# Kernel tuning notes

Measured on AMD Instinct MI355X. Metric: run time of the kernel, lower is better.

The kernel has to match this reference:

```python
import jax, jax.numpy as jnp
import numpy as np

NUM_OBS_OS = 8
NUM_OBS_TS = 6
HIDDEN = 128
NUM_ACTIONS = 9
B = 32768
N_TS = 32


def setup_inputs() -> dict:
    key = jax.random.key(0)
    ks = jax.random.split(key, 16)
    s_OS = jax.random.normal(ks[0], (B, NUM_OBS_OS), dtype=jnp.float32)
    s_TS = jax.random.normal(ks[1], (B, N_TS, NUM_OBS_TS), dtype=jnp.float32)
    # variable number of valid target ships per row (0..N_TS); trailing slots -> NaN
    lengths = jax.random.randint(ks[2], (B,), 0, N_TS + 1)
    pad = jnp.arange(N_TS)[None, :] >= lengths[:, None]          # [B, N_TS]
    s_TS = jnp.where(pad[:, :, None], jnp.nan, s_TS)
    s = jnp.concatenate([s_OS, s_TS.reshape(B, N_TS * NUM_OBS_TS)], axis=1)

    def lin(k, out_d, in_d):
        bound = 1.0 / np.sqrt(in_d)
        kw, kb = jax.random.split(k)
        W = jax.random.uniform(kw, (out_d, in_d), jnp.float32, -bound, bound)
        b = jax.random.uniform(kb, (out_d,), jnp.float32, -bound, bound)
        return W, b

    W_os, b_os = lin(ks[3], HIDDEN, NUM_OBS_OS)
    bound = 1.0 / np.sqrt(HIDDEN)
    W_ih = jax.random.uniform(ks[4], (4 * HIDDEN, NUM_OBS_TS), jnp.float32, -bound, bound)
    W_hh = jax.random.uniform(ks[5], (4 * HIDDEN, HIDDEN), jnp.float32, -bound, bound)
    b_ih = jax.random.uniform(ks[6], (4 * HIDDEN,), jnp.float32, -bound, bound)
    b_hh = jax.random.uniform(ks[7], (4 * HIDDEN,), jnp.float32, -bound, bound)
    W_ts, b_ts = lin(ks[8], HIDDEN, HIDDEN)
    W_c1, b_c1 = lin(ks[9], HIDDEN, 2 * HIDDEN)
    W_c2, b_c2 = lin(ks[10], NUM_ACTIONS, HIDDEN)
    return {"s": s, "W_os": W_os, "b_os": b_os, "W_ih": W_ih, "W_hh": W_hh,
            "b_ih": b_ih, "b_hh": b_hh, "W_ts": W_ts, "b_ts": b_ts,
            "W_c1": W_c1, "b_c1": b_c1, "W_c2": W_c2, "b_c2": b_c2}


def _lstm(x, W_ih, W_hh, b_ih, b_hh):
    """Single-layer batch-first LSTM; x: [B, T, I] -> outputs [B, T, H]."""
    Bc, T, _ = x.shape
    H = W_hh.shape[1]
    # precompute input projections for all steps: [T, B, 4H]
    xg = jnp.einsum('bti,gi->tbg', x, W_ih) + (b_ih + b_hh)

    def step(carry, xt):
        h, c = carry
        gates = xt + h @ W_hh.T                      # [B, 4H]
        i, f, g, o = jnp.split(gates, 4, axis=-1)    # torch order: i, f, g, o
        i = jax.nn.sigmoid(i)
        f = jax.nn.sigmoid(f)
        g = jnp.tanh(g)
        o = jax.nn.sigmoid(o)
        c = f * c + i * g
        h = o * jnp.tanh(c)
        return (h, c), h

    h0 = jnp.zeros((Bc, H), x.dtype)
    c0 = jnp.zeros((Bc, H), x.dtype)
    _, hs = jax.lax.scan(step, (h0, c0), xg)         # hs: [T, B, H]
    return jnp.transpose(hs, (1, 0, 2))


def reference(s, W_os, b_os, W_ih, W_hh, b_ih, b_hh, W_ts, b_ts, W_c1, b_c1, W_c2, b_c2):
    Bc = s.shape[0]
    s_OS = s[:, :NUM_OBS_OS]
    s_TS = s[:, NUM_OBS_OS:].reshape(Bc, -1, NUM_OBS_TS)          # [B, N_TS, 6]
    valid = jnp.logical_not(jnp.isnan(s_TS[:, :, 0]))             # [B, N_TS]
    n_obs = jnp.sum(valid, axis=1)                                # [B]
    h_idx = jnp.maximum(n_obs, 1) - 1                             # last valid step
    s_TS = jnp.where(jnp.isnan(s_TS), 0.0, s_TS)

    x_OS = jax.nn.relu(s_OS @ W_os.T + b_os)                      # [B, 128]

    out = _lstm(s_TS, W_ih, W_hh, b_ih, b_hh)                     # [B, N_TS, 128]
    x_TS = jnp.take_along_axis(out, h_idx[:, None, None], axis=1)[:, 0]  # [B, 128]
    x_TS = jnp.where((n_obs == 0)[:, None], 0.0, x_TS)
    x_TS = jax.nn.relu(x_TS @ W_ts.T + b_ts)

    x = jnp.concatenate([x_OS, x_TS], axis=1)                     # [B, 256]
    x = jax.nn.relu(x @ W_c1.T + b_c1)
    return x @ W_c2.T + b_c2                                      # [B, num_actions]
```

## Files before the change

kernel.cpp:

```cpp
#include <hip/hip_runtime.h>

#define NOBS_OS 8
#define NOBS_TS 6
#define HID 128
#define NACT 9
#define BTOT 32768
#define NTS 32
#define ROWS 16
#define NTILES 2048
#define QUADS 512
#define BLOCK 512
#define PREB 128

#define LEN_OFF 0
#define PERM_OFF BTOT
#define HIST_OFF (2 * BTOT)

typedef __attribute__((ext_vector_type(8))) short short8;
typedef __attribute__((ext_vector_type(4))) float f32x4;

__device__ inline unsigned pkbf(float a, float b) {
  unsigned r;
  asm("v_cvt_pk_bf16_f32 %0, %1, %2" : "=v"(r) : "v"(a), "v"(b));
  return r;
}

__device__ inline float fexp2(float x) {
#if defined(__has_builtin) && __has_builtin(__builtin_amdgcn_exp2f)
  return __builtin_amdgcn_exp2f(x);
#else
  return exp2f(x);
#endif
}
__device__ inline float frcp_(float x) {
#if defined(__has_builtin) && __has_builtin(__builtin_amdgcn_rcpf)
  return __builtin_amdgcn_rcpf(x);
#else
  return 1.0f / x;
#endif
}

__device__ inline short8 pack8(f32x4 a, f32x4 b) {
  union { unsigned u[4]; short8 s; } r;
  r.u[0] = pkbf(a[0], a[1]); r.u[1] = pkbf(a[2], a[3]);
  r.u[2] = pkbf(b[0], b[1]); r.u[3] = pkbf(b[2], b[3]);
  return r.s;
}

__device__ inline short8 pack8s(const float* p, float s) {
  union { unsigned u[4]; short8 r; } r;
#pragma unroll
  for (int i = 0; i < 4; ++i) r.u[i] = pkbf(p[2 * i] * s, p[2 * i + 1] * s);
  return r.r;
}

__global__ void count_kernel(const float* __restrict__ s, int* __restrict__ ws) {
  __shared__ int lh[NTS + 1];
  const int tid = threadIdx.x;
  if (tid <= NTS) lh[tid] = 0;
  __syncthreads();
  const int row = blockIdx.x * 256 + tid;
  const float* p = s + (size_t)row * 200 + NOBS_OS;
  int lo = 0, hi = NTS;
  while (lo < hi) {
    const int mid = (lo + hi) >> 1;
    const float v = p[mid * NOBS_TS];
    if (v == v) lo = mid + 1; else hi = mid;
  }
  ws[LEN_OFF + row] = lo;
  atomicAdd(&lh[lo], 1);
  __syncthreads();
  if (tid <= NTS) ws[HIST_OFF + blockIdx.x * (NTS + 1) + tid] = lh[tid];
}

__global__ void scatter_kernel(int* __restrict__ ws) {
  __shared__ int tot[NTS + 1], pre[NTS + 1], gb[NTS + 1], lh[NTS + 1];
  const int tid = threadIdx.x;
  if (tid <= NTS) {
    int t = 0, pr = 0;
    for (int k = 0; k < PREB; ++k) {
      const int h = ws[HIST_OFF + k * (NTS + 1) + tid];
      t += h;
      if (k < (int)blockIdx.x) pr += h;
    }
    tot[tid] = t;
    pre[tid] = pr;
    lh[tid] = 0;
  }
  __syncthreads();
  if (tid == 0) {
    int a = 0;
    for (int b = 0; b <= NTS; ++b) { gb[b] = a; a += tot[b]; }
  }
  __syncthreads();
  const int row = blockIdx.x * 256 + tid;
  const int len = ws[LEN_OFF + row];
  const int r = atomicAdd(&lh[len], 1);
  __syncthreads();
  ws[PERM_OFF + gb[len] + pre[len] + r] = row;
}


#define GX(CN, T)                                                            \
  {                                                                          \
    short8 ax = z8;                                                          \
    if (q == 0) ax = *(const short8*)&x_st[CN][c * 264 + (T) * 8];           \
    _Pragma("unroll") for (int a = 0; a < 4; ++a)                            \
        acc[CN][a] = __builtin_amdgcn_mfma_f32_16x16x32_bf16(                \
            ax, Bh[a][4], biasv[a], 0, 0, 0);                                \
  }

#define GH(CN, T)                                                            \
  {                                                                          \
    const unsigned short* hb = hA[CN][((T) + 1) & 1];                        \
    _Pragma("unroll") for (int kt = 0; kt < 4; ++kt) {                       \
      const short8 ah = *(const short8*)&hb[kt * 512 + L * 8];               \
      _Pragma("unroll") for (int a = 0; a < 4; ++a)                          \
          acc[CN][a] = __builtin_amdgcn_mfma_f32_16x16x32_bf16(              \
              ah, Bh[a][kt], acc[CN][a], 0, 0, 0);                           \
    }                                                                        \
  }

#define ACT(CN, T)                                                           \
  {                                                                          \
    unsigned short* hw = &hA[CN][(T) & 1][pbase];                            \
    float hv[4];                                                             \
    _Pragma("unroll") for (int r = 0; r < 4; ++r) {                          \
      const float ei = fexp2(acc[CN][0][r]);                                 \
      const float ef = fexp2(acc[CN][1][r]);                                 \
      const float eg = fexp2(acc[CN][2][r]);                                 \
      const float eo = fexp2(acc[CN][3][r]);                                 \
      const float P = (1.0f + ei) * (1.0f + eg);                             \
      const float fp = 1.0f + ef;                                            \
      const float num = cc[CN][r] * P + (1.0f - eg) * fp;                    \
      const float cv = num * frcp_(fp * P);                                  \
      cc[CN][r] = cv;                                                        \
      const float ec = fexp2(cv * -2.88539008f);                             \
      const float roc = frcp_((1.0f + eo) * (1.0f + ec));                    \
      hv[r] = (1.0f - ec) * roc;                                             \
    }                                                                        \
    const unsigned p01 = pkbf(hv[0], hv[1]);                                 \
    const unsigned p23 = pkbf(hv[2], hv[3]);                                 \
    hw[0] = (unsigned short)p01;                                             \
    hw[8] = (unsigned short)(p01 >> 16);                                     \
    hw[16] = (unsigned short)p23;                                            \
    hw[24] = (unsigned short)(p23 >> 16);                                    \
    _Pragma("unroll") for (int r = 0; r < 4; ++r) {                          \
      if (((tpck[CN] >> (r * 8)) & 255u) == (unsigned)(T))                   \
        xts[CN][r] = hv[r];                                                  \
    }                                                                        \
  }

__global__ __launch_bounds__(BLOCK, 2) void recdqn_kernel(
    const float* __restrict__ s, const float* __restrict__ W_os,
    const float* __restrict__ b_os, const float* __restrict__ W_ih,
    const float* __restrict__ W_hh, const float* __restrict__ b_ih,
    const float* __restrict__ b_hh, const float* __restrict__ W_ts,
    const float* __restrict__ b_ts, const float* __restrict__ W_c1,
    const float* __restrict__ b_c1, const float* __restrict__ W_c2,
    const float* __restrict__ b_c2, const int* __restrict__ ws,
    float* __restrict__ out) {
  __shared__ unsigned short x_st[4][ROWS * 264];
  __shared__ unsigned short hA[4][2][2048];
  __shared__ unsigned short xtsb[4][2048];
  __shared__ int n_lds[4][ROWS];
  __shared__ int rid_s[4][ROWS];
  __shared__ int tmax_sh[4];
  unsigned short* xcat_al = &hA[0][0][0];
  unsigned short* x2b_al = &xtsb[0][0];

  const int tid = threadIdx.x;
  const int L = tid & 63;
  const int w = tid >> 6;
  const int c = L & 15;
  const int q = L >> 4;
  const int j = (w << 4) | c;

  const short8 z8 = {0, 0, 0, 0, 0, 0, 0, 0};

  short8 Bh[4][5];
  f32x4 biasv[4];
#pragma unroll
  for (int a = 0; a < 4; ++a) {
    const float sc = (a == 2) ? -2.88539008f : -1.44269504f;
    const int n = (a << 7) + j;
    const float bb = sc * (b_ih[n] + b_hh[n]);
    f32x4 bv = {bb, bb, bb, bb};
    biasv[a] = bv;
#pragma unroll
    for (int kt = 0; kt < 4; ++kt)
      Bh[a][kt] = pack8s(W_hh + n * HID + kt * 32 + q * 8, sc);
    short8 fx = z8;
    if (q == 0) {
      const float* px = W_ih + n * NOBS_TS;
      union { unsigned u[4]; short8 s; } fu;
      fu.u[0] = pkbf(px[0] * sc, px[1] * sc);
      fu.u[1] = pkbf(px[2] * sc, px[3] * sc);
      fu.u[2] = pkbf(px[4] * sc, px[5] * sc);
      fu.u[3] = 0;
      fx = fu.s;
    }
    Bh[a][4] = fx;
  }

  const int pbase = ((j >> 5) << 9) + (((j >> 3) & 3) << 7) + (q << 5) + (j & 7);

  const int p = (QUADS - 1) - blockIdx.x;
  if (tid < 64) {
    const int cn = tid >> 4, rr = tid & 15;
    const int row = ws[PERM_OFF + (4 * p + cn) * ROWS + rr];
    rid_s[cn][rr] = row;
    n_lds[cn][rr] = ws[LEN_OFF + row];
  }
  __syncthreads();

#pragma unroll
  for (int it = 0; it < 4; ++it) {
    const int slot = tid + it * 512;
    const int cn = slot >> 9, rt = slot & 511, r = rt >> 5, tq = rt & 31;
    short8 v = z8;
    if (tq < n_lds[cn][r]) {
      const float2* ps =
          (const float2*)(s + (size_t)rid_s[cn][r] * 200 + NOBS_OS + tq * NOBS_TS);
      const float2 A = ps[0], Bv = ps[1], Cv = ps[2];
      union { unsigned u[4]; short8 s; } vu;
      vu.u[0] = pkbf(A.x, A.y);
      vu.u[1] = pkbf(Bv.x, Bv.y);
      vu.u[2] = pkbf(Cv.x, Cv.y);
      vu.u[3] = 0;
      v = vu.s;
    }
    *(short8*)&x_st[cn][r * 264 + tq * 8] = v;
  }
  if (tid == 0) {
#pragma unroll
    for (int cn = 0; cn < 4; ++cn) {
      int mx = 0;
      for (int r = 0; r < ROWS; ++r) mx = max(mx, n_lds[cn][r]);
      tmax_sh[cn] = mx;
    }
  }
  __syncthreads();

  const int tm0 = tmax_sh[0], tm1 = tmax_sh[1];
  const int tm2 = tmax_sh[2], tm3 = tmax_sh[3];
  unsigned tpck[4];
#pragma unroll
  for (int cn = 0; cn < 4; ++cn) {
    unsigned pk = 0;
#pragma unroll
    for (int b = 0; b < 4; ++b)
      pk |= ((unsigned)((n_lds[cn][q * 4 + b] - 1) & 255)) << (b * 8);
    tpck[cn] = pk;
  }

  float cc[4][4], xts[4][4];
#pragma unroll
  for (int i = 0; i < 4; ++i) {
    cc[0][i] = 0.0f; cc[1][i] = 0.0f; cc[2][i] = 0.0f; cc[3][i] = 0.0f;
    xts[0][i] = 0.0f; xts[1][i] = 0.0f; xts[2][i] = 0.0f; xts[3][i] = 0.0f;
  }

  f32x4 acc[4][4];
  if (tm3 > 0) {
    if (tm0 > 0) GX(0, 0)
    if (tm1 > 0) GX(1, 0)
    if (tm2 > 0) GX(2, 0)
    GX(3, 0)
    if (tm0 > 0) ACT(0, 0)
    if (tm1 > 0) ACT(1, 0)
    if (tm2 > 0) ACT(2, 0)
    ACT(3, 0)
    __syncthreads();
    int t = 1;
    for (; t < tm0; ++t) {
      GX(0, t) GH(0, t)
      GX(1, t) GH(1, t)
      GX(2, t) GH(2, t)
      GX(3, t) GH(3, t)
      ACT(0, t) ACT(1, t) ACT(2, t) ACT(3, t)
      __syncthreads();
    }
    for (; t < tm1; ++t) {
      GX(1, t) GH(1, t)
      GX(2, t) GH(2, t)
      GX(3, t) GH(3, t)
      ACT(1, t) ACT(2, t) ACT(3, t)
      __syncthreads();
    }
    for (; t < tm2; ++t) {
      GX(2, t) GH(2, t)
      GX(3, t) GH(3, t)
      ACT(2, t) ACT(3, t)
      __syncthreads();
    }
    for (; t < tm3; ++t) {
      GX(3, t) GH(3, t)
      ACT(3, t)
      __syncthreads();
    }
  }

#pragma unroll
  for (int cn = 0; cn < 4; ++cn) {
    const unsigned p01 = pkbf(xts[cn][0], xts[cn][1]);
    const unsigned p23 = pkbf(xts[cn][2], xts[cn][3]);
    unsigned short* pw = &xtsb[cn][pbase];
    pw[0] = (unsigned short)p01;
    pw[8] = (unsigned short)(p01 >> 16);
    pw[16] = (unsigned short)p23;
    pw[24] = (unsigned short)(p23 >> 16);
  }
  __syncthreads();

  short8 Fts[4], Fc1[8], Fc2[4], bosf = z8;
#pragma unroll
  for (int kt = 0; kt < 4; ++kt) {
    const f32x4* pp = (const f32x4*)(W_ts + j * HID + kt * 32 + q * 8);
    Fts[kt] = pack8(pp[0], pp[1]);
  }
#pragma unroll
  for (int kt = 0; kt < 8; ++kt) {
    const f32x4* pp = (const f32x4*)(W_c1 + j * 256 + kt * 32 + q * 8);
    Fc1[kt] = pack8(pp[0], pp[1]);
  }
#pragma unroll
  for (int kt = 0; kt < 4; ++kt) Fc2[kt] = z8;
  if (w == 0 && c < NACT) {
#pragma unroll
    for (int kt = 0; kt < 4; ++kt) {
      const f32x4* pp = (const f32x4*)(W_c2 + c * HID + kt * 32 + q * 8);
      Fc2[kt] = pack8(pp[0], pp[1]);
    }
  }
  if (q == 0) {
    const f32x4* pb = (const f32x4*)(W_os + j * NOBS_OS);
    bosf = pack8(pb[0], pb[1]);
  }
  const float bts = b_ts[j], bc1 = b_c1[j], bos = b_os[j];
  const float bc2 = (w == 0 && c < NACT) ? b_c2[c] : 0.0f;

#pragma unroll
  for (int cn = 0; cn < 4; ++cn) {
    f32x4 a2 = {bts, bts, bts, bts};
#pragma unroll
    for (int kt = 0; kt < 4; ++kt) {
      const short8 af = *(const short8*)&xtsb[cn][kt * 512 + L * 8];
      a2 = __builtin_amdgcn_mfma_f32_16x16x32_bf16(af, Fts[kt], a2, 0, 0, 0);
    }
    const unsigned p01 = pkbf(fmaxf(a2[0], 0.0f), fmaxf(a2[1], 0.0f));
    const unsigned p23 = pkbf(fmaxf(a2[2], 0.0f), fmaxf(a2[3], 0.0f));
    unsigned short* xc = xcat_al + cn * 4096 + 2048 + pbase;
    xc[0] = (unsigned short)p01;
    xc[8] = (unsigned short)(p01 >> 16);
    xc[16] = (unsigned short)p23;
    xc[24] = (unsigned short)(p23 >> 16);
  }
#pragma unroll
  for (int cn = 0; cn < 4; ++cn) {
    short8 aos = z8;
    if (q == 0) {
      const f32x4* pa = (const f32x4*)(s + (size_t)rid_s[cn][c] * 200);
      aos = pack8(pa[0], pa[1]);
    }
    f32x4 a2 = {bos, bos, bos, bos};
    a2 = __builtin_amdgcn_mfma_f32_16x16x32_bf16(aos, bosf, a2, 0, 0, 0);
    const unsigned p01 = pkbf(fmaxf(a2[0], 0.0f), fmaxf(a2[1], 0.0f));
    const unsigned p23 = pkbf(fmaxf(a2[2], 0.0f), fmaxf(a2[3], 0.0f));
    unsigned short* xc = xcat_al + cn * 4096 + pbase;
    xc[0] = (unsigned short)p01;
    xc[8] = (unsigned short)(p01 >> 16);
    xc[16] = (unsigned short)p23;
    xc[24] = (unsigned short)(p23 >> 16);
  }
  __syncthreads();

#pragma unroll
  for (int cn = 0; cn < 4; ++cn) {
    f32x4 a2 = {bc1, bc1, bc1, bc1};
#pragma unroll
    for (int kt = 0; kt < 8; ++kt) {
      const short8 af = *(const short8*)&xcat_al[cn * 4096 + kt * 512 + L * 8];
      a2 = __builtin_amdgcn_mfma_f32_16x16x32_bf16(af, Fc1[kt], a2, 0, 0, 0);
    }
    const unsigned p01 = pkbf(fmaxf(a2[0], 0.0f), fmaxf(a2[1], 0.0f));
    const unsigned p23 = pkbf(fmaxf(a2[2], 0.0f), fmaxf(a2[3], 0.0f));
    unsigned short* xb = x2b_al + cn * 2048 + pbase;
    xb[0] = (unsigned short)p01;
    xb[8] = (unsigned short)(p01 >> 16);
    xb[16] = (unsigned short)p23;
    xb[24] = (unsigned short)(p23 >> 16);
  }
  __syncthreads();

  if (w == 0) {
#pragma unroll
    for (int cn = 0; cn < 4; ++cn) {
      f32x4 accf = {bc2, bc2, bc2, bc2};
#pragma unroll
      for (int kt = 0; kt < 4; ++kt) {
        const short8 af = *(const short8*)&x2b_al[cn * 2048 + kt * 512 + L * 8];
        accf = __builtin_amdgcn_mfma_f32_16x16x32_bf16(af, Fc2[kt], accf, 0, 0, 0);
      }
      if (c < NACT) {
#pragma unroll
        for (int r = 0; r < 4; ++r)
          out[(size_t)rid_s[cn][q * 4 + r] * NACT + c] = accf[r];
      }
    }
  }
}

extern "C" void kernel_launch(void* const* d_in, const int* in_sizes, int n_in,
                              void* d_out, int out_size, void* d_ws, size_t ws_size,
                              hipStream_t stream) {
  (void)in_sizes; (void)n_in; (void)out_size; (void)ws_size;
  const float* s    = (const float*)d_in[0];
  const float* W_os = (const float*)d_in[1];
  const float* b_os = (const float*)d_in[2];
  const float* W_ih = (const float*)d_in[3];
  const float* W_hh = (const float*)d_in[4];
  const float* b_ih = (const float*)d_in[5];
  const float* b_hh = (const float*)d_in[6];
  const float* W_ts = (const float*)d_in[7];
  const float* b_ts = (const float*)d_in[8];
  const float* W_c1 = (const float*)d_in[9];
  const float* b_c1 = (const float*)d_in[10];
  const float* W_c2 = (const float*)d_in[11];
  const float* b_c2 = (const float*)d_in[12];
  int* ws = (int*)d_ws;
  float* outp = (float*)d_out;

  count_kernel<<<PREB, 256, 0, stream>>>(s, ws);
  scatter_kernel<<<PREB, 256, 0, stream>>>(ws);
  recdqn_kernel<<<QUADS, BLOCK, 0, stream>>>(
      s, W_os, b_os, W_ih, W_hh, b_ih, b_hh, W_ts, b_ts, W_c1, b_c1, W_c2,
      b_c2, ws, outp);
}
```

Before: 231.6 us.

## Run eight interleaved LSTM chains per block and stream inputs from global

```diff
diff --git a/kernel.cpp b/kernel.cpp
--- a/kernel.cpp
+++ b/kernel.cpp
@@ -8,7 +8,8 @@
 #define NTS 32
 #define ROWS 16
 #define NTILES 2048
-#define QUADS 512
+#define CHAINS 8
+#define GRID 256
 #define BLOCK 512
 #define PREB 128
 
@@ -101,24 +102,51 @@
 }
 
 
-#define GX(CN, T)                                                            \
+#define GXL(CN, T)                                                           \
   {                                                                          \
-    short8 ax = z8;                                                          \
-    if (q == 0) ax = *(const short8*)&x_st[CN][c * 264 + (T) * 8];           \
-    _Pragma("unroll") for (int a = 0; a < 4; ++a)                            \
-        acc[CN][a] = __builtin_amdgcn_mfma_f32_16x16x32_bf16(                \
-            ax, Bh[a][4], biasv[a], 0, 0, 0);                                \
-  }
-
-#define GH(CN, T)                                                            \
+    axv##CN = z8;                                                            \
+    if (q == 0) {                                                            \
+      const float2* ps =                                                     \
+          (const float2*)(s + (size_t)ridr[CN] * 200 + NOBS_OS + (T) * NOBS_TS); \
+      const float2 A = ps[0], Bv = ps[1], Cv = ps[2];                        \
+      union { unsigned u[4]; short8 s8; } vu;                                \
+      vu.u[0] = pkbf(A.x, A.y);                                              \
+      vu.u[1] = pkbf(Bv.x, Bv.y);                                            \
+      vu.u[2] = pkbf(Cv.x, Cv.y);                                            \
+      vu.u[3] = 0;                                                           \
+      axv##CN = vu.s8;                                                       \
+    }                                                                        \
+  }
+
+#define GHF(CN, T)                                                           \
   {                                                                          \
     const unsigned short* hb = hA[CN][((T) + 1) & 1];                        \
-    _Pragma("unroll") for (int kt = 0; kt < 4; ++kt) {                       \
+    {                                                                        \
+      const short8 ah = *(const short8*)&hb[L * 8];                          \
+      _Pragma("unroll") for (int a = 0; a < 4; ++a)                          \
+          acc[(CN) & 3][a] = __builtin_amdgcn_mfma_f32_16x16x32_bf16(        \
+              ah, Bh[a][0], biasv[a], 0, 0, 0);                              \
+    }                                                                        \
+    _Pragma("unroll") for (int kt = 1; kt < 4; ++kt) {                       \
       const short8 ah = *(const short8*)&hb[kt * 512 + L * 8];               \
       _Pragma("unroll") for (int a = 0; a < 4; ++a)                          \
-          acc[CN][a] = __builtin_amdgcn_mfma_f32_16x16x32_bf16(              \
-              ah, Bh[a][kt], acc[CN][a], 0, 0, 0);                           \
+          acc[(CN) & 3][a] = __builtin_amdgcn_mfma_f32_16x16x32_bf16(        \
+              ah, Bh[a][kt], acc[(CN) & 3][a], 0, 0, 0);                     \
     }                                                                        \
+  }
+
+#define GXM(CN)                                                              \
+  {                                                                          \
+    _Pragma("unroll") for (int a = 0; a < 4; ++a)                            \
+        acc[(CN) & 3][a] = __builtin_amdgcn_mfma_f32_16x16x32_bf16(          \
+            axv##CN, Bh[a][4], acc[(CN) & 3][a], 0, 0, 0);                   \
+  }
+
+#define GX0(CN)                                                              \
+  {                                                                          \
+    _Pragma("unroll") for (int a = 0; a < 4; ++a)                            \
+        acc[(CN) & 3][a] = __builtin_amdgcn_mfma_f32_16x16x32_bf16(          \
+            axv##CN, Bh[a][4], biasv[a], 0, 0, 0);                           \
   }
 
 #define ACT(CN, T)                                                           \
@@ -126,10 +154,10 @@
     unsigned short* hw = &hA[CN][(T) & 1][pbase];                            \
     float hv[4];                                                             \
     _Pragma("unroll") for (int r = 0; r < 4; ++r) {                          \
-      const float ei = fexp2(acc[CN][0][r]);                                 \
-      const float ef = fexp2(acc[CN][1][r]);                                 \
-      const float eg = fexp2(acc[CN][2][r]);                                 \
-      const float eo = fexp2(acc[CN][3][r]);                                 \
+      const float ei = fexp2(acc[(CN) & 3][0][r]);                           \
+      const float ef = fexp2(acc[(CN) & 3][1][r]);                           \
+      const float eg = fexp2(acc[(CN) & 3][2][r]);                           \
+      const float eo = fexp2(acc[(CN) & 3][3][r]);                           \
       const float P = (1.0f + ei) * (1.0f + eg);                             \
       const float fp = 1.0f + ef;                                            \
       const float num = cc[CN][r] * P + (1.0f - eg) * fp;                    \
@@ -141,14 +169,19 @@
     }                                                                        \
     const unsigned p01 = pkbf(hv[0], hv[1]);                                 \
     const unsigned p23 = pkbf(hv[2], hv[3]);                                 \
-    hw[0] = (unsigned short)p01;                                             \
-    hw[8] = (unsigned short)(p01 >> 16);                                     \
-    hw[16] = (unsigned short)p23;                                            \
-    hw[24] = (unsigned short)(p23 >> 16);                                    \
-    _Pragma("unroll") for (int r = 0; r < 4; ++r) {                          \
-      if (((tpck[CN] >> (r * 8)) & 255u) == (unsigned)(T))                   \
-        xts[CN][r] = hv[r];                                                  \
-    }                                                                        \
+    const unsigned short hb16_0 = (unsigned short)p01;                       \
+    const unsigned short hb16_1 = (unsigned short)(p01 >> 16);               \
+    const unsigned short hb16_2 = (unsigned short)p23;                       \
+    const unsigned short hb16_3 = (unsigned short)(p23 >> 16);               \
+    hw[0] = hb16_0;                                                          \
+    hw[8] = hb16_1;                                                          \
+    hw[16] = hb16_2;                                                         \
+    hw[24] = hb16_3;                                                         \
+    unsigned short* xw = &xtsb[CN][pbase];                                   \
+    if (((tpck[CN] >> 0) & 255u) == (unsigned)(T)) xw[0] = hb16_0;           \
+    if (((tpck[CN] >> 8) & 255u) == (unsigned)(T)) xw[8] = hb16_1;           \
+    if (((tpck[CN] >> 16) & 255u) == (unsigned)(T)) xw[16] = hb16_2;         \
+    if (((tpck[CN] >> 24) & 255u) == (unsigned)(T)) xw[24] = hb16_3;         \
   }
 
 __global__ __launch_bounds__(BLOCK, 2) void recdqn_kernel(
@@ -160,12 +193,11 @@
     const float* __restrict__ b_c1, const float* __restrict__ W_c2,
     const float* __restrict__ b_c2, const int* __restrict__ ws,
     float* __restrict__ out) {
-  __shared__ unsigned short x_st[4][ROWS * 264];
-  __shared__ unsigned short hA[4][2][2048];
-  __shared__ unsigned short xtsb[4][2048];
-  __shared__ int n_lds[4][ROWS];
-  __shared__ int rid_s[4][ROWS];
-  __shared__ int tmax_sh[4];
+  __shared__ unsigned short hA[CHAINS][2][2048];
+  __shared__ unsigned short xtsb[CHAINS][2048];
+  __shared__ int n_lds[CHAINS][ROWS];
+  __shared__ int rid_s[CHAINS][ROWS];
+  __shared__ int tmax_sh[CHAINS];
   unsigned short* xcat_al = &hA[0][0][0];
   unsigned short* x2b_al = &xtsb[0][0];
 
@@ -193,125 +225,98 @@
     short8 fx = z8;
     if (q == 0) {
       const float* px = W_ih + n * NOBS_TS;
-      union { unsigned u[4]; short8 s; } fu;
+      union { unsigned u[4]; short8 s8; } fu;
       fu.u[0] = pkbf(px[0] * sc, px[1] * sc);
       fu.u[1] = pkbf(px[2] * sc, px[3] * sc);
       fu.u[2] = pkbf(px[4] * sc, px[5] * sc);
       fu.u[3] = 0;
-      fx = fu.s;
+      fx = fu.s8;
     }
     Bh[a][4] = fx;
   }
 
   const int pbase = ((j >> 5) << 9) + (((j >> 3) & 3) << 7) + (q << 5) + (j & 7);
 
-  const int p = (QUADS - 1) - blockIdx.x;
-  if (tid < 64) {
+  if (tid < CHAINS * ROWS) {
     const int cn = tid >> 4, rr = tid & 15;
-    const int row = ws[PERM_OFF + (4 * p + cn) * ROWS + rr];
+    const int row = ws[PERM_OFF + ((int)blockIdx.x + 256 * cn) * ROWS + rr];
     rid_s[cn][rr] = row;
     n_lds[cn][rr] = ws[LEN_OFF + row];
   }
-  __syncthreads();
-
-#pragma unroll
-  for (int it = 0; it < 4; ++it) {
-    const int slot = tid + it * 512;
-    const int cn = slot >> 9, rt = slot & 511, r = rt >> 5, tq = rt & 31;
-    short8 v = z8;
-    if (tq < n_lds[cn][r]) {
-      const float2* ps =
-          (const float2*)(s + (size_t)rid_s[cn][r] * 200 + NOBS_OS + tq * NOBS_TS);
-      const float2 A = ps[0], Bv = ps[1], Cv = ps[2];
-      union { unsigned u[4]; short8 s; } vu;
-      vu.u[0] = pkbf(A.x, A.y);
-      vu.u[1] = pkbf(Bv.x, Bv.y);
-      vu.u[2] = pkbf(Cv.x, Cv.y);
-      vu.u[3] = 0;
-      v = vu.s;
-    }
-    *(short8*)&x_st[cn][r * 264 + tq * 8] = v;
-  }
-  if (tid == 0) {
-#pragma unroll
-    for (int cn = 0; cn < 4; ++cn) {
-      int mx = 0;
-      for (int r = 0; r < ROWS; ++r) mx = max(mx, n_lds[cn][r]);
-      tmax_sh[cn] = mx;
-    }
-  }
-  __syncthreads();
-
-  const int tm0 = tmax_sh[0], tm1 = tmax_sh[1];
-  const int tm2 = tmax_sh[2], tm3 = tmax_sh[3];
-  unsigned tpck[4];
-#pragma unroll
-  for (int cn = 0; cn < 4; ++cn) {
+  {
+    short8* xz = (short8*)&xtsb[0][0];
+#pragma unroll
+    for (int i2 = 0; i2 < 4; ++i2) xz[tid + i2 * 512] = z8;
+  }
+  __syncthreads();
+  if (tid < CHAINS) {
+    int mx = 0;
+    for (int r = 0; r < ROWS; ++r) mx = max(mx, n_lds[tid][r]);
+    tmax_sh[tid] = mx;
+  }
+  __syncthreads();
+
+  const int tm0 = tmax_sh[0], tm1 = tmax_sh[1], tm2 = tmax_sh[2],
+            tm3 = tmax_sh[3], tm4 = tmax_sh[4], tm5 = tmax_sh[5],
+            tm6 = tmax_sh[6], tm7 = tmax_sh[7];
+  unsigned tpck[CHAINS];
+  int ridr[CHAINS];
+#pragma unroll
+  for (int cn = 0; cn < CHAINS; ++cn) {
     unsigned pk = 0;
 #pragma unroll
     for (int b = 0; b < 4; ++b)
       pk |= ((unsigned)((n_lds[cn][q * 4 + b] - 1) & 255)) << (b * 8);
     tpck[cn] = pk;
-  }
-
-  float cc[4][4], xts[4][4];
-#pragma unroll
-  for (int i = 0; i < 4; ++i) {
-    cc[0][i] = 0.0f; cc[1][i] = 0.0f; cc[2][i] = 0.0f; cc[3][i] = 0.0f;
-    xts[0][i] = 0.0f; xts[1][i] = 0.0f; xts[2][i] = 0.0f; xts[3][i] = 0.0f;
-  }
+    ridr[cn] = rid_s[cn][c];
+  }
+
+  float cc[CHAINS][4];
+#pragma unroll
+  for (int cn = 0; cn < CHAINS; ++cn)
+#pragma unroll
+    for (int i = 0; i < 4; ++i) cc[cn][i] = 0.0f;
 
   f32x4 acc[4][4];
-  if (tm3 > 0) {
-    if (tm0 > 0) GX(0, 0)
-    if (tm1 > 0) GX(1, 0)
-    if (tm2 > 0) GX(2, 0)
-    GX(3, 0)
+  short8 axv0, axv1, axv2, axv3, axv4, axv5, axv6, axv7;
+  if (tm7 > 0) {
+    if (tm0 > 0) { GXL(0, 0) GX0(0) }
+    if (tm1 > 0) { GXL(1, 0) GX0(1) }
+    if (tm2 > 0) { GXL(2, 0) GX0(2) }
+    if (tm3 > 0) { GXL(3, 0) GX0(3) }
     if (tm0 > 0) ACT(0, 0)
     if (tm1 > 0) ACT(1, 0)
     if (tm2 > 0) ACT(2, 0)
-    ACT(3, 0)
+    if (tm3 > 0) ACT(3, 0)
+    if (tm4 > 0) { GXL(4, 0) GX0(4) }
+    if (tm5 > 0) { GXL(5, 0) GX0(5) }
+    if (tm6 > 0) { GXL(6, 0) GX0(6) }
+    { GXL(7, 0) GX0(7) }
+    if (tm4 > 0) ACT(4, 0)
+    if (tm5 > 0) ACT(5, 0)
+    if (tm6 > 0) ACT(6, 0)
+    ACT(7, 0)
     __syncthreads();
-    int t = 1;
-    for (; t < tm0; ++t) {
-      GX(0, t) GH(0, t)
-      GX(1, t) GH(1, t)
-      GX(2, t) GH(2, t)
-      GX(3, t) GH(3, t)
-      ACT(0, t) ACT(1, t) ACT(2, t) ACT(3, t)
+    for (int t = 1; t < tm7; ++t) {
+      if (t < tm0) { GXL(0, t) GHF(0, t) GXM(0) }
+      if (t < tm1) { GXL(1, t) GHF(1, t) GXM(1) }
+      if (t < tm2) { GXL(2, t) GHF(2, t) GXM(2) }
+      if (t < tm3) { GXL(3, t) GHF(3, t) GXM(3) }
+      if (t < tm0) ACT(0, t)
+      if (t < tm1) ACT(1, t)
+      if (t < tm2) ACT(2, t)
+      if (t < tm3) ACT(3, t)
+      if (t < tm4) { GXL(4, t) GHF(4, t) GXM(4) }
+      if (t < tm5) { GXL(5, t) GHF(5, t) GXM(5) }
+      if (t < tm6) { GXL(6, t) GHF(6, t) GXM(6) }
+      { GXL(7, t) GHF(7, t) GXM(7) }
+      if (t < tm4) ACT(4, t)
+      if (t < tm5) ACT(5, t)
+      if (t < tm6) ACT(6, t)
+      ACT(7, t)
       __syncthreads();
     }
-    for (; t < tm1; ++t) {
-      GX(1, t) GH(1, t)
-      GX(2, t) GH(2, t)
-      GX(3, t) GH(3, t)
-      ACT(1, t) ACT(2, t) ACT(3, t)
-      __syncthreads();
-    }
-    for (; t < tm2; ++t) {
-      GX(2, t) GH(2, t)
-      GX(3, t) GH(3, t)
-      ACT(2, t) ACT(3, t)
-      __syncthreads();
-    }
-    for (; t < tm3; ++t) {
-      GX(3, t) GH(3, t)
-      ACT(3, t)
-      __syncthreads();
-    }
-  }
-
-#pragma unroll
-  for (int cn = 0; cn < 4; ++cn) {
-    const unsigned p01 = pkbf(xts[cn][0], xts[cn][1]);
-    const unsigned p23 = pkbf(xts[cn][2], xts[cn][3]);
-    unsigned short* pw = &xtsb[cn][pbase];
-    pw[0] = (unsigned short)p01;
-    pw[8] = (unsigned short)(p01 >> 16);
-    pw[16] = (unsigned short)p23;
-    pw[24] = (unsigned short)(p23 >> 16);
-  }
-  __syncthreads();
+  }
 
   short8 Fts[4], Fc1[8], Fc2[4], bosf = z8;
 #pragma unroll
@@ -341,7 +346,7 @@
   const float bc2 = (w == 0 && c < NACT) ? b_c2[c] : 0.0f;
 
 #pragma unroll
-  for (int cn = 0; cn < 4; ++cn) {
+  for (int cn = 0; cn < CHAINS; ++cn) {
     f32x4 a2 = {bts, bts, bts, bts};
 #pragma unroll
     for (int kt = 0; kt < 4; ++kt) {
@@ -357,7 +362,7 @@
     xc[24] = (unsigned short)(p23 >> 16);
   }
 #pragma unroll
-  for (int cn = 0; cn < 4; ++cn) {
+  for (int cn = 0; cn < CHAINS; ++cn) {
     short8 aos = z8;
     if (q == 0) {
       const f32x4* pa = (const f32x4*)(s + (size_t)rid_s[cn][c] * 200);
@@ -376,7 +381,7 @@
   __syncthreads();
 
 #pragma unroll
-  for (int cn = 0; cn < 4; ++cn) {
+  for (int cn = 0; cn < CHAINS; ++cn) {
     f32x4 a2 = {bc1, bc1, bc1, bc1};
 #pragma unroll
     for (int kt = 0; kt < 8; ++kt) {
@@ -395,7 +400,7 @@
 
   if (w == 0) {
 #pragma unroll
-    for (int cn = 0; cn < 4; ++cn) {
+    for (int cn = 0; cn < CHAINS; ++cn) {
       f32x4 accf = {bc2, bc2, bc2, bc2};
 #pragma unroll
       for (int kt = 0; kt < 4; ++kt) {
@@ -433,7 +438,7 @@
 
   count_kernel<<<PREB, 256, 0, stream>>>(s, ws);
   scatter_kernel<<<PREB, 256, 0, stream>>>(ws);
-  recdqn_kernel<<<QUADS, BLOCK, 0, stream>>>(
+  recdqn_kernel<<<GRID, BLOCK, 0, stream>>>(
       s, W_os, b_os, W_ih, W_hh, b_ih, b_hh, W_ts, b_ts, W_c1, b_c1, W_c2,
       b_c2, ws, outp);
 }
```

Result: slower. 262.7 us (+13.4%).
